# Optimization experiments

Hardware: AMD Instinct MI355X
Metric: run time of the kernel (lower is better)

## Reference

```python
import jax, jax.numpy as jnp
import numpy as np

B, NF, DIM, H, W = 2, 8, 128, 40, 40
HID = 256
INNER = 2 * HID            # expansion=2
QKB = 4                    # qkv_block_size -> head dim
NH = INNER // QKB          # 128 heads
DH = QKB                   # 4


def _layernorm(x, w, b, eps=1e-5):
    mu = x.mean(-1, keepdims=True)
    var = x.var(-1, keepdims=True)
    return (x - mu) / jnp.sqrt(var + eps) * w + b


def _mlstm(q, k, v, ig, fg):
    # q,k,v: (Bp,NH,S,DH); ig,fg: (Bp,NH,S,1). Parallel stabilized mLSTM.
    S = q.shape[2]
    lfc = jnp.cumsum(jax.nn.log_sigmoid(fg), axis=2)            # (Bp,NH,S,1)
    m = lfc - jnp.swapaxes(lfc, -2, -1)                          # (Bp,NH,S,S): lfc[i]-lfc[j]
    tri = jnp.tril(jnp.ones((S, S), dtype=bool))
    logD = jnp.where(tri, m + jnp.swapaxes(ig, -2, -1), -jnp.inf)
    maxD = jnp.max(logD, axis=-1, keepdims=True)
    Dm = jnp.exp(logD - maxD)
    qk = jnp.einsum('bnsd,bntd->bnst', q, k) / jnp.sqrt(jnp.asarray(DH, q.dtype))
    C = qk * Dm
    normalizer = jnp.maximum(jnp.abs(C.sum(-1, keepdims=True)), jnp.exp(-maxD))
    return jnp.einsum('bnst,bntd->bnsd', C / (normalizer + 1e-6), v)


def _vil_layer(x, up_w, up_b, conv_w, conv_b, q_w, k_w, ig_w, ig_b, fg_w, fg_b, onorm_w, onorm_b, skip, down_w, down_b):
    Bp, S, _ = x.shape
    xz = x @ up_w.T + up_b                                       # (Bp,S,2*INNER)
    xm, z = jnp.split(xz, 2, axis=-1)
    # causal depthwise conv1d, kernel 4, left pad 3
    xc = jax.lax.conv_general_dilated(jnp.swapaxes(xm, 1, 2), conv_w[:, None, :], (1,), [(3, 0)],
                                      dimension_numbers=('NCH', 'OIH', 'NCH'), feature_group_count=INNER)
    xa = jax.nn.silu(jnp.swapaxes(xc, 1, 2) + conv_b)            # (Bp,S,INNER)
    xah = xa.reshape(Bp, S, NH, DH)
    qh = jnp.einsum('bsnd,ned->bsne', xah, q_w)                  # headwise linear (no bias)
    kh = jnp.einsum('bsnd,ned->bsne', xah, k_w)
    gate_in = jnp.concatenate([qh.reshape(Bp, S, INNER), kh.reshape(Bp, S, INNER), xm], axis=-1)
    ig = jnp.swapaxes(gate_in @ ig_w.T + ig_b, 1, 2)[..., None]  # (Bp,NH,S,1)
    fg = jnp.swapaxes(gate_in @ fg_w.T + fg_b, 1, 2)[..., None]
    q = jnp.swapaxes(qh, 1, 2)
    k = jnp.swapaxes(kh, 1, 2)
    v = jnp.swapaxes(xm.reshape(Bp, S, NH, DH), 1, 2)
    h = _mlstm(q, k, v, ig, fg)                                  # (Bp,NH,S,DH)
    mu = h.mean(-1, keepdims=True)
    var = h.var(-1, keepdims=True)
    hn = (h - mu) / jnp.sqrt(var + 1e-5) * onorm_w.reshape(NH, DH)[None, :, None, :] + onorm_b.reshape(NH, DH)[None, :, None, :]
    h_flat = jnp.swapaxes(hn, 1, 2).reshape(Bp, S, INNER)
    hs = h_flat + skip * xa
    return (hs * jax.nn.silu(z)) @ down_w.T + down_b


def _forward(x, in_fc1_w, in_fc1_b, in_fc2_w, in_fc2_b, out_fc1_w, out_fc1_b, out_fc2_w, out_fc2_b,
             norm_w, norm_b, up_w, up_b, conv_w, conv_b, q_w, k_w, ig_w, ig_b, fg_w, fg_b,
             onorm_w, onorm_b, skip, down_w, down_b):
    Bv, nf, C, Hh, Ww = x.shape
    x_flat = jnp.transpose(x, (0, 3, 4, 1, 2)).reshape(Bv * Hh * Ww, nf, C)
    h = jax.nn.gelu(x_flat @ in_fc1_w.T + in_fc1_b, approximate=False)
    h = h @ in_fc2_w.T + in_fc2_b
    # ViLBlockPair: forward-direction block then backward (flipped) block, each pre-LN residual
    for i, flip in ((0, False), (1, True)):
        y = _layernorm(h, norm_w[i], norm_b[i])
        if flip:
            y = y[:, ::-1]
        y = _vil_layer(y, up_w[i], up_b[i], conv_w[i], conv_b[i], q_w[i], k_w[i], ig_w[i], ig_b[i],
                       fg_w[i], fg_b[i], onorm_w[i], onorm_b[i], skip[i], down_w[i], down_b[i])
        if flip:
            y = y[:, ::-1]
        h = h + y
    o = jax.nn.gelu(h @ out_fc1_w.T + out_fc1_b, approximate=False)
    o = o @ out_fc2_w.T + out_fc2_b
    out = x_flat + o
    return jnp.transpose(out.reshape(Bv, Hh, Ww, nf, C), (0, 3, 4, 1, 2))


def setup_inputs() -> dict:
    key = jax.random.key(0)
    ks = jax.random.split(key, 16)

    def rn(k, shape, std=0.02):
        return jax.random.normal(k, shape, jnp.float32) * std

    return {
        'x': jax.random.normal(ks[0], (B, NF, DIM, H, W), jnp.float32),
        'in_fc1_w': rn(ks[1], (DIM, DIM)), 'in_fc1_b': jnp.zeros((DIM,), jnp.float32),
        'in_fc2_w': rn(ks[2], (HID, DIM)), 'in_fc2_b': jnp.zeros((HID,), jnp.float32),
        'out_fc1_w': rn(ks[3], (HID, HID)), 'out_fc1_b': jnp.zeros((HID,), jnp.float32),
        'out_fc2_w': rn(ks[4], (DIM, HID)), 'out_fc2_b': jnp.zeros((DIM,), jnp.float32),
        'norm_w': jnp.ones((2, HID), jnp.float32), 'norm_b': jnp.zeros((2, HID), jnp.float32),
        'up_w': rn(ks[5], (2, 2 * INNER, HID)), 'up_b': jnp.zeros((2, 2 * INNER), jnp.float32),
        'conv_w': rn(ks[6], (2, INNER, 4), 0.1), 'conv_b': jnp.zeros((2, INNER), jnp.float32),
        'q_w': rn(ks[7], (2, NH, DH, DH), 0.1), 'k_w': rn(ks[8], (2, NH, DH, DH), 0.1),
        'ig_w': rn(ks[9], (2, NH, 3 * INNER), 0.01), 'ig_b': rn(ks[10], (2, NH), 0.1),
        'fg_w': rn(ks[11], (2, NH, 3 * INNER), 0.01),
        'fg_b': jnp.tile(jnp.linspace(3.0, 6.0, NH, dtype=jnp.float32)[None], (2, 1)),
        'onorm_w': jnp.ones((2, INNER), jnp.float32), 'onorm_b': jnp.zeros((2, INNER), jnp.float32),
        'skip': jnp.ones((2, INNER), jnp.float32),
        'down_w': rn(ks[12], (2, HID, INNER)), 'down_b': jnp.zeros((2, HID), jnp.float32),
    }


def reference(x, in_fc1_w, in_fc1_b, in_fc2_w, in_fc2_b, out_fc1_w, out_fc1_b, out_fc2_w, out_fc2_b,
              norm_w, norm_b, up_w, up_b, conv_w, conv_b, q_w, k_w, ig_w, ig_b, fg_w, fg_b,
              onorm_w, onorm_b, skip, down_w, down_b):
    return _forward(x, in_fc1_w, in_fc1_b, in_fc2_w, in_fc2_b, out_fc1_w, out_fc1_b, out_fc2_w, out_fc2_b,
                    norm_w, norm_b, up_w, up_b, conv_w, conv_b, q_w, k_w, ig_w, ig_b, fg_w, fg_b,
                    onorm_w, onorm_b, skip, down_w, down_b)
```

## Files before the change

### kernel.cpp

```cpp
#include <hip/hip_runtime.h>
#include <cstddef>
#include <cstdint>


#define NPOS 3200
#define MTOK 25600

typedef __attribute__((ext_vector_type(8))) short short8;
typedef __attribute__((ext_vector_type(8))) unsigned short u16x8;
typedef __attribute__((ext_vector_type(4))) float f32x4;

__device__ __forceinline__ float bf2f(unsigned short u) {
  union { uint32_t i; float f; } v; v.i = ((uint32_t)u) << 16; return v.f;
}
__device__ __forceinline__ unsigned short f2bf(float f) {
  union { float f; uint32_t i; } v; v.f = f;
  uint32_t r = (v.i + 0x7fffu + ((v.i >> 16) & 1u)) >> 16;
  return (unsigned short)r;
}
__device__ __forceinline__ float geluf(float x) {
  return 0.5f * x * (1.0f + erff(x * 0.70710678118654752f));
}
__device__ __forceinline__ float fast_rcp(float x) { return __builtin_amdgcn_rcpf(x); }
__device__ __forceinline__ float silu_fast(float x) {
  return x * fast_rcp(1.0f + __expf(-x));
}

#define OFF_FC1 0
#define OFF_FC2 16384
#define OFF_OFC1 49152
#define OFF_OFC2 114688
#define OFF_UP 147456
#define OFF_DW 671744
#define OFF_GW 933888
#define WB_ELEMS 1458176

__global__ __launch_bounds__(256) void wprep(const float* __restrict__ fc1w,
                                             const float* __restrict__ fc2w,
                                             const float* __restrict__ ofc1w,
                                             const float* __restrict__ ofc2w,
                                             const float* __restrict__ upw,
                                             const float* __restrict__ dww,
                                             const float* __restrict__ igw,
                                             const float* __restrict__ fgw,
                                             const float* __restrict__ qw,
                                             const float* __restrict__ kw,
                                             const float* __restrict__ igbias,
                                             const float* __restrict__ fgbias,
                                             unsigned short* __restrict__ wb,
                                             float* __restrict__ gbias) {
  int i = blockIdx.x * 256 + threadIdx.x;
  if (i < 16384) { wb[OFF_FC1 + i] = f2bf(fc1w[i]); return; }
  i -= 16384;
  if (i < 32768) { wb[OFF_FC2 + i] = f2bf(fc2w[i]); return; }
  i -= 32768;
  if (i < 65536) { wb[OFF_OFC1 + i] = f2bf(ofc1w[i]); return; }
  i -= 65536;
  if (i < 32768) { wb[OFF_OFC2 + i] = f2bf(ofc2w[i]); return; }
  i -= 32768;
  if (i < 524288) { wb[OFF_UP + i] = f2bf(upw[i]); return; }
  i -= 524288;
  if (i < 262144) { wb[OFF_DW + i] = f2bf(dww[i]); return; }
  i -= 262144;
  if (i < 262144) {
    const int l = i >> 17;
    const int r = i & 131071;
    const int gate = r >> 16;
    const int rr = r & 65535;
    const int row = rr >> 9, c = rr & 511;
    const float* src = (gate ? fgw : igw) + (size_t)l * 196608 + (size_t)row * 1536 + 1024 + c;
    wb[OFF_GW + (size_t)l * 262144 + (size_t)(2 * row + gate) * 1024 + 512 + c] = f2bf(*src);
    return;
  }
  i -= 262144;
  if (i < 131072) {
    const int l = i >> 16;
    const int r = i & 65535;
    const int jj = r >> 9, c = r & 511;
    const int n = c >> 2, d = c & 3;
    const float* igp = igw + (size_t)l * 196608;
    const float* fgp = fgw + (size_t)l * 196608;
    const float* qp = qw + l * 2048;
    const float* kp = kw + l * 2048;
    float si = 0.f, sf = 0.f;
#pragma unroll
    for (int e = 0; e < 4; ++e) {
      const float qv = qp[n * 16 + e * 4 + d];
      const float kv = kp[n * 16 + e * 4 + d];
      si += igp[jj * 1536 + n * 4 + e] * qv + igp[jj * 1536 + 512 + n * 4 + e] * kv;
      sf += fgp[jj * 1536 + n * 4 + e] * qv + fgp[jj * 1536 + 512 + n * 4 + e] * kv;
    }
    wb[OFF_GW + (size_t)l * 262144 + (size_t)(2 * jj) * 1024 + c] = f2bf(si);
    wb[OFF_GW + (size_t)l * 262144 + (size_t)(2 * jj + 1) * 1024 + c] = f2bf(sf);
    return;
  }
  i -= 131072;
  if (i < 512) {
    const int l = i >> 8, c = i & 255;
    gbias[l * 256 + c] = (c & 1) ? fgbias[l * 128 + (c >> 1)] : igbias[l * 128 + (c >> 1)];
  }
}

__global__ __launch_bounds__(256) void trans_in(const float* __restrict__ x,
                                                unsigned short* __restrict__ xf) {
  __shared__ float tile[32][33];
  const int b = blockIdx.z;
  const int hw0 = blockIdx.x * 32;
  const int sc0 = blockIdx.y * 32;
  const int tx = threadIdx.x, ty = threadIdx.y;
#pragma unroll
  for (int i = 0; i < 32; i += 8)
    tile[ty + i][tx] = x[((size_t)b * 1024 + sc0 + ty + i) * 1600 + hw0 + tx];
  __syncthreads();
#pragma unroll
  for (int i = 0; i < 32; i += 8)
    xf[((size_t)b * 1600 + hw0 + ty + i) * 1024 + sc0 + tx] = f2bf(tile[tx][ty + i]);
}

__global__ __launch_bounds__(256) void trans_out(const float* __restrict__ x,
                                                 const unsigned short* __restrict__ o,
                                                 float* __restrict__ out) {
  __shared__ float tile[32][33];
  const int b = blockIdx.z;
  const int hw0 = blockIdx.x * 32;
  const int sc0 = blockIdx.y * 32;
  const int tx = threadIdx.x, ty = threadIdx.y;
#pragma unroll
  for (int i = 0; i < 32; i += 8)
    tile[ty + i][tx] = bf2f(o[((size_t)b * 1600 + hw0 + ty + i) * 1024 + sc0 + tx]);
  __syncthreads();
#pragma unroll
  for (int i = 0; i < 32; i += 8) {
    size_t idx = ((size_t)b * 1024 + sc0 + ty + i) * 1600 + hw0 + tx;
    out[idx] = x[idx] + tile[tx][ty + i];
  }
}

template <int MODE>
__global__ __launch_bounds__(256) void mgemm(const unsigned short* __restrict__ A, int lda,
                                             const unsigned short* __restrict__ A2, int lda2,
                                             int KA,
                                             const unsigned short* __restrict__ W, int ldw,
                                             const float* __restrict__ bias,
                                             const unsigned short* __restrict__ Cin,
                                             void* __restrict__ Cv, int ldc, int K,
                                             int flip) {
  __shared__ __align__(16) unsigned short Als[2][4][128][8];
  __shared__ __align__(16) unsigned short Bls[2][4][128][8];
  const int t = threadIdx.x;
  const int lane = t & 63, wid = t >> 6;
  const int wr = wid >> 1, wc = wid & 1;
  const int nwg = gridDim.x * gridDim.y;
  const int bid = blockIdx.y * gridDim.x + blockIdx.x;
  const int q = nwg >> 3, r = nwg & 7;
  const int xcd = bid & 7, idx = bid >> 3;
  const int swz = (xcd < r ? xcd * (q + 1) : r * (q + 1) + (xcd - r) * q) + idx;
  const int bx = swz & (gridDim.x - 1);
  const int by = swz >> (31 - __builtin_clz(gridDim.x));
  const int bm = by * 128, bn = bx * 128;
  const int srow = t >> 1;
  const int skh = (t & 1) << 4;
  const int ch = skh >> 3;
  const int kc = lane >> 4;
  const int lr = lane & 15;
  f32x4 acc[4][4] = {};
  const unsigned short* Wp = W + (size_t)(bn + srow) * ldw + skh;

  auto gload = [&](int k0, u16x8& a0, u16x8& a1, u16x8& b0, u16x8& b1) {
    const unsigned short* Ab;
    int kk, ldA;
    if (k0 < KA) { Ab = A; kk = k0; ldA = lda; }
    else { Ab = A2; kk = k0 - KA; ldA = lda2; }
    const unsigned short* ap = Ab + (size_t)(bm + srow) * ldA + kk + skh;
    a0 = *(const u16x8*)ap;
    a1 = *(const u16x8*)(ap + 8);
    b0 = *(const u16x8*)(Wp + k0);
    b1 = *(const u16x8*)(Wp + k0 + 8);
  };
  auto swrite = [&](int buf, u16x8 a0, u16x8 a1, u16x8 b0, u16x8 b1) {
    *(u16x8*)&Als[buf][ch][srow][0] = a0;
    *(u16x8*)&Als[buf][ch + 1][srow][0] = a1;
    *(u16x8*)&Bls[buf][ch][srow][0] = b0;
    *(u16x8*)&Bls[buf][ch + 1][srow][0] = b1;
  };

  u16x8 ca0, ca1, cb0, cb1;
  gload(0, ca0, ca1, cb0, cb1);
  swrite(0, ca0, ca1, cb0, cb1);
  if (K > 32) gload(32, ca0, ca1, cb0, cb1);
  __syncthreads();
  int cur = 0;
  for (int k0 = 0; k0 < K; k0 += 32) {
    u16x8 na0, na1, nb0, nb1;
    if (k0 + 64 < K) gload(k0 + 64, na0, na1, nb0, nb1);
    short8 af[4], bf[4];
#pragma unroll
    for (int mi = 0; mi < 4; ++mi)
      af[mi] = *(const short8*)&Als[cur][kc][wr * 64 + mi * 16 + lr][0];
#pragma unroll
    for (int ni = 0; ni < 4; ++ni)
      bf[ni] = *(const short8*)&Bls[cur][kc][wc * 64 + ni * 16 + lr][0];
#pragma unroll
    for (int mi = 0; mi < 4; ++mi)
#pragma unroll
      for (int ni = 0; ni < 4; ++ni)
        acc[mi][ni] = __builtin_amdgcn_mfma_f32_16x16x32_bf16(af[mi], bf[ni], acc[mi][ni], 0, 0, 0);
    if (k0 + 32 < K) swrite(cur ^ 1, ca0, ca1, cb0, cb1);
    __syncthreads();
    ca0 = na0; ca1 = na1; cb0 = nb0; cb1 = nb1;
    cur ^= 1;
  }

#pragma unroll
  for (int mi = 0; mi < 4; ++mi) {
#pragma unroll
    for (int j = 0; j < 4; ++j) {
      const int m = bm + wr * 64 + mi * 16 + (lane >> 4) * 4 + j;
#pragma unroll
      for (int ni = 0; ni < 4; ++ni) {
        const int col = bn + wc * 64 + ni * 16 + lr;
        float v = acc[mi][ni][j] + bias[col];
        if (MODE == 1) v = geluf(v);
        if (MODE == 0 || MODE == 1) {
          ((unsigned short*)Cv)[(size_t)m * ldc + col] = f2bf(v);
        } else if (MODE == 2) {
          const int pq = m >> 3, s = m & 7;
          const int fs = flip ? (7 - s) : s;
          unsigned short* p = (unsigned short*)Cv + (size_t)(pq * 8 + fs) * ldc + col;
          *p = f2bf(bf2f(*p) + v);
        } else {
          const int pq = m >> 3, s = m & 7;
          const int fs = flip ? (7 - s) : s;
          const size_t ix = (size_t)(pq * 8 + fs) * ldc + col;
          ((unsigned short*)Cv)[ix] = f2bf(bf2f(Cin[ix]) + v);
        }
      }
    }
  }
}

__global__ __launch_bounds__(256) void ln_k(const unsigned short* __restrict__ h,
                                            const float* __restrict__ w,
                                            const float* __restrict__ b,
                                            unsigned short* __restrict__ y, int flip) {
  const int m = blockIdx.x * 4 + (threadIdx.x >> 6);
  const int lane = threadIdx.x & 63;
  const int p = m >> 3, s = m & 7;
  const int ss = flip ? (7 - s) : s;
  const unsigned short* row = h + (size_t)(p * 8 + ss) * 256;
  ushort4 u4 = *(const ushort4*)(row + lane * 4);
  float v0 = bf2f(u4.x), v1 = bf2f(u4.y), v2 = bf2f(u4.z), v3 = bf2f(u4.w);
  float sum = v0 + v1 + v2 + v3;
  float sq = v0 * v0 + v1 * v1 + v2 * v2 + v3 * v3;
#pragma unroll
  for (int o = 32; o > 0; o >>= 1) {
    sum += __shfl_xor(sum, o);
    sq += __shfl_xor(sq, o);
  }
  float mu = sum * (1.f / 256.f);
  float var = sq * (1.f / 256.f) - mu * mu;
  float r = rsqrtf(var + 1e-5f);
  float4 wv = *(const float4*)(w + lane * 4);
  float4 bv = *(const float4*)(b + lane * 4);
  ushort4 o_;
  o_.x = f2bf((v0 - mu) * r * wv.x + bv.x);
  o_.y = f2bf((v1 - mu) * r * wv.y + bv.y);
  o_.z = f2bf((v2 - mu) * r * wv.z + bv.z);
  o_.w = f2bf((v3 - mu) * r * wv.w + bv.w);
  *(ushort4*)(y + (size_t)m * 256 + lane * 4) = o_;
}

__global__ __launch_bounds__(512) void conv_k(const unsigned short* __restrict__ xz,
                                              const float* __restrict__ cw,
                                              const float* __restrict__ cb,
                                              unsigned short* __restrict__ xa) {
  const int p = blockIdx.x;
  const int c = threadIdx.x;
  float v[8];
#pragma unroll
  for (int s = 0; s < 8; ++s) v[s] = bf2f(xz[(size_t)(p * 8 + s) * 1024 + c]);
  const float4 cwv = *(const float4*)(cw + c * 4);
  const float cbv = cb[c];
#pragma unroll
  for (int s = 0; s < 8; ++s) {
    float acc = cbv + v[s] * cwv.w;
    if (s >= 1) acc += v[s - 1] * cwv.z;
    if (s >= 2) acc += v[s - 2] * cwv.y;
    if (s >= 3) acc += v[s - 3] * cwv.x;
    xa[(size_t)(p * 8 + s) * 512 + c] = f2bf(silu_fast(acc));
  }
}

__global__ __launch_bounds__(256) void mlstm_k(unsigned short* __restrict__ xab,
                                               const unsigned short* __restrict__ xz,
                                               const unsigned short* __restrict__ gateb,
                                               const float* __restrict__ cw,
                                               const float* __restrict__ cb,
                                               const float* __restrict__ qw,
                                               const float* __restrict__ kw,
                                               const float* __restrict__ onw,
                                               const float* __restrict__ onb,
                                               const float* __restrict__ skp) {
  const int p = blockIdx.x * 2 + (threadIdx.x >> 7);
  const int n = threadIdx.x & 127;
  float kwv[4][4], cwt[4][4];
  float cbv[4];
#pragma unroll
  for (int e = 0; e < 4; ++e) {
    float4 k4 = *(const float4*)(kw + n * 16 + e * 4);
    kwv[e][0] = k4.x; kwv[e][1] = k4.y; kwv[e][2] = k4.z; kwv[e][3] = k4.w;
    float4 c4 = *(const float4*)(cw + (n * 4 + e) * 4);
    cwt[e][0] = c4.x; cwt[e][1] = c4.y; cwt[e][2] = c4.z; cwt[e][3] = c4.w;
  }
  {
    float4 cb4 = *(const float4*)(cb + n * 4);
    cbv[0] = cb4.x; cbv[1] = cb4.y; cbv[2] = cb4.z; cbv[3] = cb4.w;
  }
  float xa[8][4], k[8][4], v[8][4], lfc[8], ig[8];
  float run = 0.f;
#pragma unroll
  for (int s = 0; s < 8; ++s) {
    const size_t row = (size_t)(p * 8 + s);
    ushort4 v4 = *(const ushort4*)(xz + row * 1024 + n * 4);
    v[s][0] = bf2f(v4.x); v[s][1] = bf2f(v4.y); v[s][2] = bf2f(v4.z); v[s][3] = bf2f(v4.w);
#pragma unroll
    for (int e = 0; e < 4; ++e) {
      float a = cbv[e] + v[s][e] * cwt[e][3];
      if (s >= 1) a += v[s - 1][e] * cwt[e][2];
      if (s >= 2) a += v[s - 2][e] * cwt[e][1];
      if (s >= 3) a += v[s - 3][e] * cwt[e][0];
      xa[s][e] = bf2f(f2bf(silu_fast(a)));
    }
#pragma unroll
    for (int e = 0; e < 4; ++e)
      k[s][e] = xa[s][0] * kwv[e][0] + xa[s][1] * kwv[e][1] + xa[s][2] * kwv[e][2] + xa[s][3] * kwv[e][3];
    const ushort2 g2 = *(const ushort2*)(gateb + row * 256 + n * 2);
    ig[s] = bf2f(g2.x);
    const float f = bf2f(g2.y);
    const float ls = fminf(f, 0.f) - __logf(1.0f + __expf(-fabsf(f)));
    run += ls;
    lfc[s] = run;
  }
  float qwv[4][4];
#pragma unroll
  for (int e = 0; e < 4; ++e) {
    float4 q4 = *(const float4*)(qw + n * 16 + e * 4);
    qwv[e][0] = q4.x; qwv[e][1] = q4.y; qwv[e][2] = q4.z; qwv[e][3] = q4.w;
  }
  const float4 onwv = *(const float4*)(onw + n * 4);
  const float4 onbv = *(const float4*)(onb + n * 4);
  const float4 skv = *(const float4*)(skp + n * 4);
#pragma unroll
  for (int s = 0; s < 8; ++s) {
    float q0, q1, q2, q3;
    q0 = xa[s][0] * qwv[0][0] + xa[s][1] * qwv[0][1] + xa[s][2] * qwv[0][2] + xa[s][3] * qwv[0][3];
    q1 = xa[s][0] * qwv[1][0] + xa[s][1] * qwv[1][1] + xa[s][2] * qwv[1][2] + xa[s][3] * qwv[1][3];
    q2 = xa[s][0] * qwv[2][0] + xa[s][1] * qwv[2][1] + xa[s][2] * qwv[2][2] + xa[s][3] * qwv[2][3];
    q3 = xa[s][0] * qwv[3][0] + xa[s][1] * qwv[3][1] + xa[s][2] * qwv[3][2] + xa[s][3] * qwv[3][3];
    float mx = -1e30f;
#pragma unroll
    for (int t = 0; t < 8; ++t)
      if (t <= s) mx = fmaxf(mx, lfc[s] - lfc[t] + ig[t]);
    float csum = 0.f;
    float o0 = 0, o1 = 0, o2 = 0, o3 = 0;
#pragma unroll
    for (int t = 0; t < 8; ++t)
      if (t <= s) {
        const float dm = __expf(lfc[s] - lfc[t] + ig[t] - mx);
        const float qkd = (q0 * k[t][0] + q1 * k[t][1] + q2 * k[t][2] + q3 * k[t][3]) * 0.5f;
        const float cc = qkd * dm;
        csum += cc;
        o0 += cc * v[t][0]; o1 += cc * v[t][1]; o2 += cc * v[t][2]; o3 += cc * v[t][3];
      }
    const float inv = fast_rcp(fmaxf(fabsf(csum), __expf(-mx)) + 1e-6f);
    o0 *= inv; o1 *= inv; o2 *= inv; o3 *= inv;
    const float mu = 0.25f * (o0 + o1 + o2 + o3);
    const float d0 = o0 - mu, d1 = o1 - mu, d2 = o2 - mu, d3 = o3 - mu;
    const float var = 0.25f * (d0 * d0 + d1 * d1 + d2 * d2 + d3 * d3);
    const float r = __builtin_amdgcn_rsqf(var + 1e-5f);
    const size_t row = (size_t)(p * 8 + s);
    ushort4 z4 = *(const ushort4*)(xz + row * 1024 + 512 + n * 4);
    ushort4 ge;
    ge.x = f2bf((d0 * r * onwv.x + onbv.x + skv.x * xa[s][0]) * silu_fast(bf2f(z4.x)));
    ge.y = f2bf((d1 * r * onwv.y + onbv.y + skv.y * xa[s][1]) * silu_fast(bf2f(z4.y)));
    ge.z = f2bf((d2 * r * onwv.z + onbv.z + skv.z * xa[s][2]) * silu_fast(bf2f(z4.z)));
    ge.w = f2bf((d3 * r * onwv.w + onbv.w + skv.w * xa[s][3]) * silu_fast(bf2f(z4.w)));
    *(ushort4*)(xab + row * 512 + n * 4) = ge;
  }
}

extern "C" void kernel_launch(void* const* d_in, const int* in_sizes, int n_in,
                              void* d_out, int out_size, void* d_ws, size_t ws_size,
                              hipStream_t stream) {
  const float* x = (const float*)d_in[0];
  const float* fc1w = (const float*)d_in[1];
  const float* fc1b = (const float*)d_in[2];
  const float* fc2w = (const float*)d_in[3];
  const float* fc2b = (const float*)d_in[4];
  const float* ofc1w = (const float*)d_in[5];
  const float* ofc1b = (const float*)d_in[6];
  const float* ofc2w = (const float*)d_in[7];
  const float* ofc2b = (const float*)d_in[8];
  const float* nw = (const float*)d_in[9];
  const float* nb = (const float*)d_in[10];
  const float* upw = (const float*)d_in[11];
  const float* upb = (const float*)d_in[12];
  const float* cw = (const float*)d_in[13];
  const float* cb = (const float*)d_in[14];
  const float* qw = (const float*)d_in[15];
  const float* kw = (const float*)d_in[16];
  const float* igw = (const float*)d_in[17];
  const float* igbias = (const float*)d_in[18];
  const float* fgw = (const float*)d_in[19];
  const float* fgbias = (const float*)d_in[20];
  const float* onw = (const float*)d_in[21];
  const float* onb = (const float*)d_in[22];
  const float* skp = (const float*)d_in[23];
  const float* dww = (const float*)d_in[24];
  const float* dwb = (const float*)d_in[25];
  float* out = (float*)d_out;

  char* ws = (char*)d_ws;
  unsigned short* hbuf = (unsigned short*)ws;
  unsigned short* bufD = (unsigned short*)(ws + 13107200);
  unsigned short* bufA = (unsigned short*)(ws + 26214400);
  unsigned short* xz = (unsigned short*)(ws + 32768000);
  unsigned short* hmirror = xz;
  unsigned short* xab = (unsigned short*)(ws + 85196800);
  unsigned short* xflat = xab;
  unsigned short* wb = (unsigned short*)(ws + 111411200);
  float* gbias = (float*)(ws + 111411200 + 2916352);

  wprep<<<dim3(5186), 256, 0, stream>>>(fc1w, fc2w, ofc1w, ofc2w, upw, dww, igw, fgw, qw, kw,
                                        igbias, fgbias, wb, gbias);

  dim3 tb(32, 8);
  trans_in<<<dim3(50, 32, 2), tb, 0, stream>>>(x, xflat);
  mgemm<1><<<dim3(1, 200), 256, 0, stream>>>(xflat, 128, xflat, 128, 128, wb + OFF_FC1, 128,
                                             fc1b, nullptr, bufA, 128, 128, 0);
  mgemm<0><<<dim3(2, 200), 256, 0, stream>>>(bufA, 128, bufA, 128, 128, wb + OFF_FC2, 128,
                                             fc2b, nullptr, hbuf, 256, 128, 0);

  for (int i = 0; i < 2; ++i) {
    ln_k<<<dim3(6400), 256, 0, stream>>>(hbuf, nw + i * 256, nb + i * 256, bufD, i);
    mgemm<0><<<dim3(8, 200), 256, 0, stream>>>(bufD, 256, bufD, 256, 256,
                                               wb + OFF_UP + (size_t)i * 262144, 256,
                                               upb + i * 1024, nullptr, xz, 1024, 256, 0);
    conv_k<<<dim3(NPOS), 512, 0, stream>>>(xz, cw + i * 2048, cb + i * 512, xab);
    mgemm<0><<<dim3(2, 200), 256, 0, stream>>>(xab, 512, xz, 1024, 512,
                                               wb + OFF_GW + (size_t)i * 262144, 1024,
                                               gbias + i * 256, nullptr, bufD, 256, 1024, 0);
    mlstm_k<<<dim3(1600), 256, 0, stream>>>(xab, xz, bufD, cw + i * 2048, cb + i * 512,
                                            qw + i * 2048, kw + i * 2048,
                                            onw + i * 512, onb + i * 512, skp + i * 512);
    if (i == 0) {
      mgemm<2><<<dim3(2, 200), 256, 0, stream>>>(xab, 512, xab, 512, 512, wb + OFF_DW, 512,
                                                 dwb, nullptr, hbuf, 256, 512, 0);
    } else {
      mgemm<6><<<dim3(2, 200), 256, 0, stream>>>(xab, 512, xab, 512, 512, wb + OFF_DW + 131072,
                                                 512, dwb + 256, hbuf, hmirror, 256, 512, 1);
    }
  }

  mgemm<1><<<dim3(2, 200), 256, 0, stream>>>(hmirror, 256, hmirror, 256, 256, wb + OFF_OFC1, 256,
                                             ofc1b, nullptr, bufD, 256, 256, 0);
  mgemm<0><<<dim3(1, 200), 256, 0, stream>>>(bufD, 256, bufD, 256, 256, wb + OFF_OFC2, 256,
                                             ofc2b, nullptr, bufA, 128, 256, 0);
  trans_out<<<dim3(50, 32, 2), tb, 0, stream>>>(x, bufA, out);
}
```

Before: 304.7 us.

## Fuse causal conv+SiLU into up-projection GEMM epilogue; drop mLSTM max stabilization

Adds a GEMM epilogue mode that writes the up-projection output and, for the xm half, computes the causal depthwise conv and SiLU in place. It uses lane shuffles to fetch the previous rows of each 8-step sequence, which removes the separate conv kernel launch and its re-read of xz. Separately, the mLSTM kernel no longer computes a per-row max for stabilization. It precomputes exp(ig - cumlogf) and exp(-cumlogf) per step, so the O(S²) exponentials become O(S). Dropping the max subtraction risks overflow or underflow when gate values are large, and the algebraic rewrite relies on the short sequence length of 8.

```diff
diff --git a/kernel.cpp b/kernel.cpp
--- a/kernel.cpp
+++ b/kernel.cpp
@@ -144,7 +144,10 @@
                                              const float* __restrict__ bias,
                                              const unsigned short* __restrict__ Cin,
                                              void* __restrict__ Cv, int ldc, int K,
-                                             int flip) {
+                                             int flip,
+                                             unsigned short* __restrict__ xa_out,
+                                             const float* __restrict__ cwp,
+                                             const float* __restrict__ cbp) {
   __shared__ __align__(16) unsigned short Als[2][4][128][8];
   __shared__ __align__(16) unsigned short Bls[2][4][128][8];
   const int t = threadIdx.x;
@@ -211,6 +214,46 @@
     cur ^= 1;
   }
 
+  if (MODE == 8) {
+    const bool isxm = (bn < 512);
+#pragma unroll
+    for (int mi = 0; mi < 4; ++mi) {
+#pragma unroll
+      for (int ni = 0; ni < 4; ++ni) {
+        const int lc = wc * 64 + ni * 16 + lr;
+        const int col = bn + lc;
+        const float bias_c = bias[col];
+        float xmv[4];
+#pragma unroll
+        for (int j = 0; j < 4; ++j) {
+          const int lm = wr * 64 + mi * 16 + (lane >> 4) * 4 + j;
+          const float v = acc[mi][ni][j] + bias_c;
+          const unsigned short bv = f2bf(v);
+          ((unsigned short*)Cv)[(size_t)(bm + lm) * ldc + col] = bv;
+          xmv[j] = bf2f(bv);
+        }
+        if (isxm) {
+          const float4 cwv = *(const float4*)(cwp + col * 4);
+          const float cbv = cbp[col];
+          const float up1 = __shfl_up(xmv[1], 16);
+          const float up2 = __shfl_up(xmv[2], 16);
+          const float up3 = __shfl_up(xmv[3], 16);
+#pragma unroll
+          for (int j = 0; j < 4; ++j) {
+            const int lm = wr * 64 + mi * 16 + (lane >> 4) * 4 + j;
+            const int s = lm & 7;
+            float a = cbv + xmv[j] * cwv.w;
+            if (s >= 1) a += (j >= 1 ? xmv[j - 1] : up3) * cwv.z;
+            if (s >= 2) a += (j >= 2 ? xmv[j - 2] : (j == 1 ? up3 : up2)) * cwv.y;
+            if (s >= 3) a += (j >= 3 ? xmv[j - 3] : (j == 2 ? up3 : (j == 1 ? up2 : up1))) * cwv.x;
+            xa_out[(size_t)(bm + lm) * 512 + col] = f2bf(silu_fast(a));
+          }
+        }
+      }
+    }
+    return;
+  }
+
 #pragma unroll
   for (int mi = 0; mi < 4; ++mi) {
 #pragma unroll
@@ -270,27 +313,6 @@
   *(ushort4*)(y + (size_t)m * 256 + lane * 4) = o_;
 }
 
-__global__ __launch_bounds__(512) void conv_k(const unsigned short* __restrict__ xz,
-                                              const float* __restrict__ cw,
-                                              const float* __restrict__ cb,
-                                              unsigned short* __restrict__ xa) {
-  const int p = blockIdx.x;
-  const int c = threadIdx.x;
-  float v[8];
-#pragma unroll
-  for (int s = 0; s < 8; ++s) v[s] = bf2f(xz[(size_t)(p * 8 + s) * 1024 + c]);
-  const float4 cwv = *(const float4*)(cw + c * 4);
-  const float cbv = cb[c];
-#pragma unroll
-  for (int s = 0; s < 8; ++s) {
-    float acc = cbv + v[s] * cwv.w;
-    if (s >= 1) acc += v[s - 1] * cwv.z;
-    if (s >= 2) acc += v[s - 2] * cwv.y;
-    if (s >= 3) acc += v[s - 3] * cwv.x;
-    xa[(size_t)(p * 8 + s) * 512 + c] = f2bf(silu_fast(acc));
-  }
-}
-
 __global__ __launch_bounds__(256) void mlstm_k(unsigned short* __restrict__ xab,
                                                const unsigned short* __restrict__ xz,
                                                const unsigned short* __restrict__ gateb,
@@ -316,7 +338,7 @@
     float4 cb4 = *(const float4*)(cb + n * 4);
     cbv[0] = cb4.x; cbv[1] = cb4.y; cbv[2] = cb4.z; cbv[3] = cb4.w;
   }
-  float xa[8][4], k[8][4], v[8][4], lfc[8], ig[8];
+  float xa[8][4], k[8][4], v[8][4], E[8], en[8];
   float run = 0.f;
 #pragma unroll
   for (int s = 0; s < 8; ++s) {
@@ -335,11 +357,12 @@
     for (int e = 0; e < 4; ++e)
       k[s][e] = xa[s][0] * kwv[e][0] + xa[s][1] * kwv[e][1] + xa[s][2] * kwv[e][2] + xa[s][3] * kwv[e][3];
     const ushort2 g2 = *(const ushort2*)(gateb + row * 256 + n * 2);
-    ig[s] = bf2f(g2.x);
+    const float igs = bf2f(g2.x);
     const float f = bf2f(g2.y);
     const float ls = fminf(f, 0.f) - __logf(1.0f + __expf(-fabsf(f)));
     run += ls;
-    lfc[s] = run;
+    E[s] = __expf(igs - run);
+    en[s] = __expf(-run);
   }
   float qwv[4][4];
 #pragma unroll
@@ -357,22 +380,17 @@
     q1 = xa[s][0] * qwv[1][0] + xa[s][1] * qwv[1][1] + xa[s][2] * qwv[1][2] + xa[s][3] * qwv[1][3];
     q2 = xa[s][0] * qwv[2][0] + xa[s][1] * qwv[2][1] + xa[s][2] * qwv[2][2] + xa[s][3] * qwv[2][3];
     q3 = xa[s][0] * qwv[3][0] + xa[s][1] * qwv[3][1] + xa[s][2] * qwv[3][2] + xa[s][3] * qwv[3][3];
-    float mx = -1e30f;
-#pragma unroll
-    for (int t = 0; t < 8; ++t)
-      if (t <= s) mx = fmaxf(mx, lfc[s] - lfc[t] + ig[t]);
     float csum = 0.f;
     float o0 = 0, o1 = 0, o2 = 0, o3 = 0;
 #pragma unroll
     for (int t = 0; t < 8; ++t)
       if (t <= s) {
-        const float dm = __expf(lfc[s] - lfc[t] + ig[t] - mx);
         const float qkd = (q0 * k[t][0] + q1 * k[t][1] + q2 * k[t][2] + q3 * k[t][3]) * 0.5f;
-        const float cc = qkd * dm;
+        const float cc = qkd * E[t];
         csum += cc;
         o0 += cc * v[t][0]; o1 += cc * v[t][1]; o2 += cc * v[t][2]; o3 += cc * v[t][3];
       }
-    const float inv = fast_rcp(fmaxf(fabsf(csum), __expf(-mx)) + 1e-6f);
+    const float inv = fast_rcp(fmaxf(fabsf(csum), en[s]) + 1e-6f);
     o0 *= inv; o1 *= inv; o2 *= inv; o3 *= inv;
     const float mu = 0.25f * (o0 + o1 + o2 + o3);
     const float d0 = o0 - mu, d1 = o1 - mu, d2 = o2 - mu, d3 = o3 - mu;
@@ -437,34 +455,41 @@
   dim3 tb(32, 8);
   trans_in<<<dim3(50, 32, 2), tb, 0, stream>>>(x, xflat);
   mgemm<1><<<dim3(1, 200), 256, 0, stream>>>(xflat, 128, xflat, 128, 128, wb + OFF_FC1, 128,
-                                             fc1b, nullptr, bufA, 128, 128, 0);
+                                             fc1b, nullptr, bufA, 128, 128, 0,
+                                             nullptr, nullptr, nullptr);
   mgemm<0><<<dim3(2, 200), 256, 0, stream>>>(bufA, 128, bufA, 128, 128, wb + OFF_FC2, 128,
-                                             fc2b, nullptr, hbuf, 256, 128, 0);
+                                             fc2b, nullptr, hbuf, 256, 128, 0,
+                                             nullptr, nullptr, nullptr);
 
   for (int i = 0; i < 2; ++i) {
     ln_k<<<dim3(6400), 256, 0, stream>>>(hbuf, nw + i * 256, nb + i * 256, bufD, i);
-    mgemm<0><<<dim3(8, 200), 256, 0, stream>>>(bufD, 256, bufD, 256, 256,
+    mgemm<8><<<dim3(8, 200), 256, 0, stream>>>(bufD, 256, bufD, 256, 256,
                                                wb + OFF_UP + (size_t)i * 262144, 256,
-                                               upb + i * 1024, nullptr, xz, 1024, 256, 0);
-    conv_k<<<dim3(NPOS), 512, 0, stream>>>(xz, cw + i * 2048, cb + i * 512, xab);
+                                               upb + i * 1024, nullptr, xz, 1024, 256, 0,
+                                               xab, cw + i * 2048, cb + i * 512);
     mgemm<0><<<dim3(2, 200), 256, 0, stream>>>(xab, 512, xz, 1024, 512,
                                                wb + OFF_GW + (size_t)i * 262144, 1024,
-                                               gbias + i * 256, nullptr, bufD, 256, 1024, 0);
+                                               gbias + i * 256, nullptr, bufD, 256, 1024, 0,
+                                               nullptr, nullptr, nullptr);
     mlstm_k<<<dim3(1600), 256, 0, stream>>>(xab, xz, bufD, cw + i * 2048, cb + i * 512,
                                             qw + i * 2048, kw + i * 2048,
                                             onw + i * 512, onb + i * 512, skp + i * 512);
     if (i == 0) {
       mgemm<2><<<dim3(2, 200), 256, 0, stream>>>(xab, 512, xab, 512, 512, wb + OFF_DW, 512,
-                                                 dwb, nullptr, hbuf, 256, 512, 0);
+                                                 dwb, nullptr, hbuf, 256, 512, 0,
+                                                 nullptr, nullptr, nullptr);
     } else {
       mgemm<6><<<dim3(2, 200), 256, 0, stream>>>(xab, 512, xab, 512, 512, wb + OFF_DW + 131072,
-                                                 512, dwb + 256, hbuf, hmirror, 256, 512, 1);
+                                                 512, dwb + 256, hbuf, hmirror, 256, 512, 1,
+                                                 nullptr, nullptr, nullptr);
     }
   }
 
   mgemm<1><<<dim3(2, 200), 256, 0, stream>>>(hmirror, 256, hmirror, 256, 256, wb + OFF_OFC1, 256,
-                                             ofc1b, nullptr, bufD, 256, 256, 0);
+                                             ofc1b, nullptr, bufD, 256, 256, 0,
+                                             nullptr, nullptr, nullptr);
   mgemm<0><<<dim3(1, 200), 256, 0, stream>>>(bufD, 256, bufD, 256, 256, wb + OFF_OFC2, 256,
-                                             ofc2b, nullptr, bufA, 128, 256, 0);
+                                             ofc2b, nullptr, bufA, 128, 256, 0,
+                                             nullptr, nullptr, nullptr);
   trans_out<<<dim3(50, 32, 2), tb, 0, stream>>>(x, bufA, out);
 }
```

Measured after the change: 314.2 us. 1.03x slower.
